# Performance work log

Hardware: AMD Instinct MI355X
Metric: run time of the kernel (lower is better)

## Reference

```python
import jax, jax.numpy as jnp
import numpy as np

BN_EPS = 1e-5

def conv1x1(x, w, b):
    # x: [B, Cin, L], w: [Cout, Cin], b: [Cout] -> [B, Cout, L]
    return jnp.einsum('bcl,oc->bol', x, w) + b[None, :, None]

def maxpool2(x):
    # x: [B, C, L] -> [B, C, L//2], kernel=stride=2
    B, C, L = x.shape
    return x.reshape(B, C, L // 2, 2).max(axis=-1)

def setup_inputs() -> dict:
    key = jax.random.key(0)
    ks = jax.random.split(key, 12)
    B, C, L = 8, 512, 4096
    Ci = C // 2
    s_in = 1.0 / np.sqrt(C)
    s_mid = 1.0 / np.sqrt(Ci)
    return {
        'x':       jax.random.normal(ks[0], (B, C, L), jnp.float32),
        'theta_w': jax.random.uniform(ks[1], (Ci, C), jnp.float32, -s_in, s_in),
        'theta_b': jax.random.uniform(ks[2], (Ci,), jnp.float32, -s_in, s_in),
        'phi_w':   jax.random.uniform(ks[3], (Ci, C), jnp.float32, -s_in, s_in),
        'phi_b':   jax.random.uniform(ks[4], (Ci,), jnp.float32, -s_in, s_in),
        'g_w':     jax.random.uniform(ks[5], (Ci, C), jnp.float32, -s_in, s_in),
        'g_b':     jax.random.uniform(ks[6], (Ci,), jnp.float32, -s_in, s_in),
        'wz_w':    jax.random.uniform(ks[7], (C, Ci), jnp.float32, -s_mid, s_mid),
        'wz_b':    jax.random.uniform(ks[8], (C,), jnp.float32, -s_mid, s_mid),
        'bn_gamma': jax.random.normal(ks[9], (C,), jnp.float32),
        'bn_beta':  jax.random.normal(ks[10], (C,), jnp.float32),
    }

def reference(x, theta_w, theta_b, phi_w, phi_b, g_w, g_b, wz_w, wz_b, bn_gamma, bn_beta):
    B, C, L = x.shape
    Ci = C // 2
    # projections
    theta = conv1x1(x, theta_w, theta_b)                 # [B, Ci, L]
    phi   = maxpool2(conv1x1(x, phi_w, phi_b))           # [B, Ci, L/2]
    g     = maxpool2(conv1x1(x, g_w, g_b))               # [B, Ci, L/2]
    # non-local attention (unscaled)
    f = jnp.einsum('bcq,bck->bqk', theta, phi)           # [B, L, L/2]
    f = jax.nn.softmax(f, axis=-1)
    y = jnp.einsum('bqk,bck->bcq', f, g)                 # [B, Ci, L]
    # wz: conv1x1 + BatchNorm1d (training mode: batch stats, biased var)
    z = conv1x1(y, wz_w, wz_b)                           # [B, C, L]
    mean = z.mean(axis=(0, 2))
    var = ((z - mean[None, :, None]) ** 2).mean(axis=(0, 2))
    z_hat = (z - mean[None, :, None]) * jax.lax.rsqrt(var + BN_EPS)[None, :, None]
    wz = z_hat * bn_gamma[None, :, None] + bn_beta[None, :, None]
    return wz + x
```

## Files before the change

### kernel.cpp

```cpp
#include <hip/hip_runtime.h>

#define BATCH 8
#define CIN   512
#define LEN   4096
#define CI    256
#define KLEN  2048

typedef _Float16 half_t;
typedef _Float16 half2_t __attribute__((ext_vector_type(2)));
typedef _Float16 half4_t __attribute__((ext_vector_type(4)));
typedef _Float16 half8_t __attribute__((ext_vector_type(8)));
typedef float    floatx4 __attribute__((ext_vector_type(4)));

__device__ __forceinline__ void async16(void* lds_dst, const void* g_src) {
    __builtin_amdgcn_global_load_lds(
        (const __attribute__((address_space(1))) unsigned int*)g_src,
        (__attribute__((address_space(3))) unsigned int*)lds_dst,
        16, 0, 0);
}

__global__ __launch_bounds__(256) void xpose_kernel(
    const float* __restrict__ x, half_t* __restrict__ xhT)
{
    __shared__ half_t tile[64][72];
    const int b = blockIdx.z, c0 = blockIdx.y * 64, l0 = blockIdx.x * 64;
    const int t = threadIdx.x;
    #pragma unroll
    for (int i = 0; i < 4; i++) {
        int fid = t + 256 * i;
        int c = fid >> 4, lb = (fid & 15) << 2;
        float4 v = *(const float4*)(x + ((size_t)b * CIN + c0 + c) * LEN + l0 + lb);
        tile[lb + 0][c] = (half_t)v.x;
        tile[lb + 1][c] = (half_t)v.y;
        tile[lb + 2][c] = (half_t)v.z;
        tile[lb + 3][c] = (half_t)v.w;
    }
    __syncthreads();
    #pragma unroll
    for (int i = 0; i < 2; i++) {
        int fid = t + 256 * i;
        int l = fid >> 3, cb = (fid & 7) << 3;
        half8_t v = *(const half8_t*)&tile[l][cb];
        *(half8_t*)(xhT + ((size_t)b * LEN + l0 + l) * CIN + c0 + cb) = v;
    }
}

__global__ __launch_bounds__(256) void wconv_kernel(
    const float* __restrict__ tw, const float* __restrict__ pw,
    const float* __restrict__ gw, const float* __restrict__ wzw,
    half_t* __restrict__ Wh, half_t* __restrict__ wzh)
{
    size_t base = ((size_t)blockIdx.x * 256 + threadIdx.x) * 8;
    const float* src;
    half_t* dst;
    if (base < 768 * 512) {
        size_t o = base >> 9, c = base & 511;
        src = (o < 256 ? tw + o * 512
                       : (o < 512 ? pw + (o - 256) * 512 : gw + (o - 512) * 512)) + c;
        dst = Wh + base;
    } else {
        size_t off = base - 768 * 512;
        src = wzw + off;
        dst = wzh + off;
    }
    float4 a = *(const float4*)src, b2 = *(const float4*)(src + 4);
    half8_t h = { (half_t)a.x, (half_t)a.y, (half_t)a.z, (half_t)a.w,
                  (half_t)b2.x, (half_t)b2.y, (half_t)b2.z, (half_t)b2.w };
    *(half8_t*)dst = h;
}

__global__ __launch_bounds__(256, 2) void projmm_kernel(
    const half_t* __restrict__ xhT, const half_t* __restrict__ Wh,
    const float* __restrict__ tb, const float* __restrict__ pb,
    const float* __restrict__ gb,
    half_t* __restrict__ thetaT, half_t* __restrict__ phiT,
    half_t* __restrict__ gH)
{
    __shared__ half_t wsm[128 * 32];
    __shared__ half_t xsm[128 * 32];

    const int b  = blockIdx.z;
    const int o0 = blockIdx.y * 128;
    const int l0 = blockIdx.x * 128;
    const int t  = threadIdx.x;
    const int lane = t & 63, w = t >> 6;
    const int ln = lane & 15, quad = lane >> 4;
    const int wm = w >> 1, wn = w & 1;

    floatx4 acc[4][4];
    #pragma unroll
    for (int mi = 0; mi < 4; mi++)
        #pragma unroll
        for (int nj = 0; nj < 4; nj++) acc[mi][nj] = (floatx4)(0.0f);

    const half_t* Wb = Wh + (size_t)o0 * 512;
    const half_t* xb = xhT + ((size_t)b * LEN + l0) * CIN;

    for (int k0 = 0; k0 < 512; k0 += 32) {
        __syncthreads();
        #pragma unroll
        for (int it = 0; it < 2; it++) {
            int off = t * 16 + it * 4096;
            int row = off >> 6, c8 = (off >> 4) & 3;
            async16(&wsm[off >> 1], Wb + (size_t)row * 512 + k0 + c8 * 8);
            async16(&xsm[off >> 1], xb + (size_t)row * CIN + k0 + c8 * 8);
        }
        __syncthreads();
        half8_t af[4], bf[4];
        #pragma unroll
        for (int mi = 0; mi < 4; mi++)
            af[mi] = *(const half8_t*)&wsm[(wm * 64 + mi * 16 + ln) * 32 + quad * 8];
        #pragma unroll
        for (int nj = 0; nj < 4; nj++)
            bf[nj] = *(const half8_t*)&xsm[(wn * 64 + nj * 16 + ln) * 32 + quad * 8];
        #pragma unroll
        for (int mi = 0; mi < 4; mi++)
            #pragma unroll
            for (int nj = 0; nj < 4; nj++)
                acc[mi][nj] = __builtin_amdgcn_mfma_f32_16x16x32_f16(
                                  af[mi], bf[nj], acc[mi][nj], 0, 0, 0);
    }

    const int which = o0 >> 8;
    const int obase = o0 & 255;
    const float* Bp = which == 0 ? tb : (which == 1 ? pb : gb);

    float bias[4][4];
    #pragma unroll
    for (int mi = 0; mi < 4; mi++)
        #pragma unroll
        for (int r = 0; r < 4; r++)
            bias[mi][r] = Bp[obase + wm * 64 + mi * 16 + quad * 4 + r];

    if (which == 0) {
        #pragma unroll
        for (int mi = 0; mi < 4; mi++) {
            int o = obase + wm * 64 + mi * 16 + quad * 4;
            #pragma unroll
            for (int nj = 0; nj < 4; nj++) {
                int l = l0 + wn * 64 + nj * 16 + ln;
                half4_t v = { (half_t)(acc[mi][nj][0] + bias[mi][0]),
                              (half_t)(acc[mi][nj][1] + bias[mi][1]),
                              (half_t)(acc[mi][nj][2] + bias[mi][2]),
                              (half_t)(acc[mi][nj][3] + bias[mi][3]) };
                *(half4_t*)(thetaT + ((size_t)b * LEN + l) * CI + o) = v;
            }
        }
    } else {
        #pragma unroll
        for (int mi = 0; mi < 4; mi++) {
            int o = obase + wm * 64 + mi * 16 + quad * 4;
            #pragma unroll
            for (int nj = 0; nj < 4; nj++) {
                int l = l0 + wn * 64 + nj * 16 + ln;
                float mx[4];
                #pragma unroll
                for (int r = 0; r < 4; r++) {
                    float other = __shfl_xor(acc[mi][nj][r], 1);
                    mx[r] = fmaxf(acc[mi][nj][r], other) + bias[mi][r];
                }
                if ((ln & 1) == 0) {
                    int kk = l >> 1;
                    if (which == 1) {
                        half4_t v = { (half_t)mx[0], (half_t)mx[1],
                                      (half_t)mx[2], (half_t)mx[3] };
                        *(half4_t*)(phiT + ((size_t)b * KLEN + kk) * CI + o) = v;
                    } else {
                        #pragma unroll
                        for (int r = 0; r < 4; r++)
                            gH[((size_t)b * CI + o + r) * KLEN + kk] = (half_t)mx[r];
                    }
                }
            }
        }
    }
}

__global__ __launch_bounds__(256, 2) void attn_kernel(
    const half_t* __restrict__ thetaT,
    const half_t* __restrict__ phiT,
    const half_t* __restrict__ gH,
    half_t* __restrict__ yhT)
{
    __shared__ half_t phi_s[64 * 256];
    __shared__ half_t g_s[256 * 64];

    const int b    = blockIdx.x;
    const int q0   = blockIdx.y * 64;
    const int t    = threadIdx.x;
    const int w    = t >> 6;
    const int lane = t & 63;
    const int ln   = lane & 15;
    const int quad = lane >> 4;
    const int qw   = q0 + w * 16;

    half8_t thf[8];
    {
        const half_t* thb = thetaT + ((size_t)b * LEN + qw + ln) * CI + quad * 8;
        #pragma unroll
        for (int ch = 0; ch < 8; ch++)
            thf[ch] = *(const half8_t*)(thb + ch * 32);
    }

    floatx4 O[16];
    #pragma unroll
    for (int i = 0; i < 16; i++) O[i] = (floatx4)(0.0f);
    float m_run = -3.0e38f;
    float l_run = 0.0f;

    const half_t* phib = phiT + (size_t)b * KLEN * CI;
    const half_t* gb   = gH   + (size_t)b * CI * KLEN;

    for (int kt = 0; kt < KLEN; kt += 64) {
        __syncthreads();
        #pragma unroll
        for (int it = 0; it < 8; it++) {
            int o   = t * 16 + it * 4096;
            int row = o >> 9;
            int gsw = (o >> 4) & 31;
            int gsrc = gsw ^ (row & 31);
            async16(&phi_s[o >> 1],
                    phib + (size_t)(kt + row) * CI + gsrc * 8);
        }
        #pragma unroll
        for (int it = 0; it < 8; it++) {
            int o   = t * 16 + it * 4096;
            int row = o >> 7;
            int gsw = (o >> 4) & 7;
            int gsrc = gsw ^ (row & 7);
            async16(&g_s[o >> 1],
                    gb + (size_t)row * KLEN + kt + gsrc * 8);
        }
        __syncthreads();

        floatx4 S[4];
        #pragma unroll
        for (int k16 = 0; k16 < 4; k16++) S[k16] = (floatx4)(0.0f);
        #pragma unroll
        for (int k16 = 0; k16 < 4; k16++) {
            int row = k16 * 16 + ln;
            int rs  = row & 31;
            #pragma unroll
            for (int ch = 0; ch < 8; ch++) {
                int gr = (ch * 4 + quad) ^ rs;
                half8_t a = *(const half8_t*)&phi_s[(row << 8) + gr * 8];
                S[k16] = __builtin_amdgcn_mfma_f32_16x16x32_f16(
                             a, thf[ch], S[k16], 0, 0, 0);
            }
        }

        float tmax = S[0][0];
        #pragma unroll
        for (int k16 = 0; k16 < 4; k16++)
            #pragma unroll
            for (int r = 0; r < 4; r++) tmax = fmaxf(tmax, S[k16][r]);
        tmax = fmaxf(tmax, __shfl_xor(tmax, 16));
        tmax = fmaxf(tmax, __shfl_xor(tmax, 32));
        float m_new = fmaxf(m_run, tmax);
        float alpha = __expf(m_run - m_new);
        m_run = m_new;
        l_run *= alpha;

        half4_t P[4];
        #pragma unroll
        for (int k16 = 0; k16 < 4; k16++) {
            float p0 = __expf(S[k16][0] - m_new);
            float p1 = __expf(S[k16][1] - m_new);
            float p2 = __expf(S[k16][2] - m_new);
            float p3 = __expf(S[k16][3] - m_new);
            l_run += (p0 + p1) + (p2 + p3);
            half4_t pv = { (half_t)p0, (half_t)p1, (half_t)p2, (half_t)p3 };
            P[k16] = pv;
        }
        #pragma unroll
        for (int i = 0; i < 16; i++) O[i] *= alpha;

        const int lnm = ln & 7;
        #pragma unroll
        for (int k16 = 0; k16 < 4; k16++) {
            int gr   = (2 * k16 + (quad >> 1)) ^ lnm;
            int coff = gr * 8 + (quad & 1) * 4;
            #pragma unroll
            for (int csub = 0; csub < 16; csub++) {
                int row = csub * 16 + ln;
                half4_t a = *(const half4_t*)&g_s[(row << 6) + coff];
                O[csub] = __builtin_amdgcn_mfma_f32_16x16x16f16(
                              a, P[k16], O[csub], 0, 0, 0);
            }
        }
    }

    l_run += __shfl_xor(l_run, 16);
    l_run += __shfl_xor(l_run, 32);
    float inv = 1.0f / l_run;
    half_t* yb = yhT + ((size_t)b * LEN + qw + ln) * CI;
    #pragma unroll
    for (int csub = 0; csub < 16; csub++) {
        int c = csub * 16 + quad * 4;
        half4_t v = { (half_t)(O[csub][0] * inv), (half_t)(O[csub][1] * inv),
                      (half_t)(O[csub][2] * inv), (half_t)(O[csub][3] * inv) };
        *(half4_t*)(yb + c) = v;
    }
}

__global__ __launch_bounds__(256, 2) void zmm_kernel(
    const half_t* __restrict__ yhT, const half_t* __restrict__ wzh,
    const float* __restrict__ wzb, float* __restrict__ z,
    float* __restrict__ bns, float* __restrict__ bnq)
{
    __shared__ half_t ysm[128 * 32];
    __shared__ half_t wsm[128 * 32];

    const int b  = blockIdx.z;
    const int o0 = blockIdx.y * 128;
    const int l0 = blockIdx.x * 128;
    const int t  = threadIdx.x;
    const int lane = t & 63, w = t >> 6;
    const int ln = lane & 15, quad = lane >> 4;
    const int wm = w >> 1, wn = w & 1;

    floatx4 acc[4][4];
    #pragma unroll
    for (int mi = 0; mi < 4; mi++)
        #pragma unroll
        for (int nj = 0; nj < 4; nj++) acc[mi][nj] = (floatx4)(0.0f);

    const half_t* yb = yhT + ((size_t)b * LEN + l0) * CI;
    const half_t* Wb = wzh + (size_t)o0 * CI;

    for (int k0 = 0; k0 < 256; k0 += 32) {
        __syncthreads();
        #pragma unroll
        for (int it = 0; it < 2; it++) {
            int off = t * 16 + it * 4096;
            int row = off >> 6, c8 = (off >> 4) & 3;
            async16(&ysm[off >> 1], yb + (size_t)row * CI + k0 + c8 * 8);
            async16(&wsm[off >> 1], Wb + (size_t)row * CI + k0 + c8 * 8);
        }
        __syncthreads();
        half8_t af[4], bf[4];
        #pragma unroll
        for (int mi = 0; mi < 4; mi++)
            af[mi] = *(const half8_t*)&ysm[(wm * 64 + mi * 16 + ln) * 32 + quad * 8];
        #pragma unroll
        for (int nj = 0; nj < 4; nj++)
            bf[nj] = *(const half8_t*)&wsm[(wn * 64 + nj * 16 + ln) * 32 + quad * 8];
        #pragma unroll
        for (int mi = 0; mi < 4; mi++)
            #pragma unroll
            for (int nj = 0; nj < 4; nj++)
                acc[mi][nj] = __builtin_amdgcn_mfma_f32_16x16x32_f16(
                                  af[mi], bf[nj], acc[mi][nj], 0, 0, 0);
    }

    float s[4] = {0, 0, 0, 0}, s2[4] = {0, 0, 0, 0};
    #pragma unroll
    for (int nj = 0; nj < 4; nj++) {
        int o = o0 + wn * 64 + nj * 16 + ln;
        float bo = wzb[o];
        #pragma unroll
        for (int mi = 0; mi < 4; mi++) {
            int l = l0 + wm * 64 + mi * 16 + quad * 4;
            float4 v = make_float4(acc[mi][nj][0] + bo, acc[mi][nj][1] + bo,
                                   acc[mi][nj][2] + bo, acc[mi][nj][3] + bo);
            *(float4*)(z + ((size_t)b * CIN + o) * LEN + l) = v;
            s[nj]  += (v.x + v.y) + (v.z + v.w);
            s2[nj] += (v.x * v.x + v.y * v.y) + (v.z * v.z + v.w * v.w);
        }
    }
    #pragma unroll
    for (int nj = 0; nj < 4; nj++) {
        float sv = s[nj], qv = s2[nj];
        sv += __shfl_xor(sv, 16); sv += __shfl_xor(sv, 32);
        qv += __shfl_xor(qv, 16); qv += __shfl_xor(qv, 32);
        if (quad == 0) {
            int o = o0 + wn * 64 + nj * 16 + ln;
            atomicAdd(&bns[o], sv);
            atomicAdd(&bnq[o], qv);
        }
    }
}

__global__ __launch_bounds__(256) void bn_kernel(
    float* __restrict__ z, const float* __restrict__ x,
    const float* __restrict__ bns, const float* __restrict__ bnq,
    const float* __restrict__ gamma, const float* __restrict__ beta)
{
    size_t i4 = (size_t)blockIdx.x * 256 + threadIdx.x;
    size_t base = i4 << 2;
    int c = (int)((base >> 12) & (CIN - 1));
    const float invn = 1.0f / (BATCH * LEN);
    float mean = bns[c] * invn;
    float var  = bnq[c] * invn - mean * mean;
    float sc = gamma[c] * rsqrtf(var + 1e-5f);
    float sh = beta[c] - mean * sc;
    float4 zv = *(const float4*)(z + base);
    float4 xv = *(const float4*)(x + base);
    float4 o;
    o.x = zv.x * sc + sh + xv.x;
    o.y = zv.y * sc + sh + xv.y;
    o.z = zv.z * sc + sh + xv.z;
    o.w = zv.w * sc + sh + xv.w;
    *(float4*)(z + base) = o;
}

extern "C" void kernel_launch(void* const* d_in, const int* in_sizes, int n_in,
                              void* d_out, int out_size, void* d_ws, size_t ws_size,
                              hipStream_t stream)
{
    const float* x     = (const float*)d_in[0];
    const float* tw    = (const float*)d_in[1];
    const float* tb    = (const float*)d_in[2];
    const float* pw    = (const float*)d_in[3];
    const float* pb    = (const float*)d_in[4];
    const float* gw    = (const float*)d_in[5];
    const float* gb    = (const float*)d_in[6];
    const float* wzw   = (const float*)d_in[7];
    const float* wzb   = (const float*)d_in[8];
    const float* gamma = (const float*)d_in[9];
    const float* beta  = (const float*)d_in[10];

    float* out = (float*)d_out;

    half_t* xhT    = (half_t*)d_ws;
    half_t* thetaT = xhT    + (size_t)BATCH * LEN * CIN;
    half_t* phiT   = thetaT + (size_t)BATCH * LEN * CI;
    half_t* gH     = phiT   + (size_t)BATCH * KLEN * CI;
    half_t* yhT    = gH     + (size_t)BATCH * CI * KLEN;
    half_t* Wh     = yhT    + (size_t)BATCH * LEN * CI;
    half_t* wzh    = Wh     + (size_t)768 * 512;
    float*  bns    = (float*)(wzh + (size_t)512 * 256);
    float*  bnq    = bns + CIN;

    hipMemsetAsync(bns, 0, 2 * CIN * sizeof(float), stream);

    wconv_kernel<<<256, 256, 0, stream>>>(tw, pw, gw, wzw, Wh, wzh);

    xpose_kernel<<<dim3(LEN / 64, CIN / 64, BATCH), 256, 0, stream>>>(x, xhT);

    projmm_kernel<<<dim3(LEN / 128, 6, BATCH), 256, 0, stream>>>(
        xhT, Wh, tb, pb, gb, thetaT, phiT, gH);

    attn_kernel<<<dim3(BATCH, LEN / 64), 256, 0, stream>>>(
        thetaT, phiT, gH, yhT);

    zmm_kernel<<<dim3(LEN / 128, CIN / 128, BATCH), 256, 0, stream>>>(
        yhT, wzh, wzb, out, bns, bnq);

    bn_kernel<<<(BATCH * CIN * LEN) / 4 / 256, 256, 0, stream>>>(
        out, x, bns, bnq, gamma, beta);
}
```

Before: 336.8 us.

## Store LDS tiles in MFMA fragment order and permute g for 16x16x32 PV

```diff
diff --git a/kernel.cpp b/kernel.cpp
--- a/kernel.cpp
+++ b/kernel.cpp
@@ -74,7 +74,7 @@
     const float* __restrict__ tb, const float* __restrict__ pb,
     const float* __restrict__ gb,
     half_t* __restrict__ thetaT, half_t* __restrict__ phiT,
-    half_t* __restrict__ gH)
+    half_t* __restrict__ gperm)
 {
     __shared__ half_t wsm[128 * 32];
     __shared__ half_t xsm[128 * 32];
@@ -100,19 +100,20 @@
         __syncthreads();
         #pragma unroll
         for (int it = 0; it < 2; it++) {
-            int off = t * 16 + it * 4096;
-            int row = off >> 6, c8 = (off >> 4) & 3;
-            async16(&wsm[off >> 1], Wb + (size_t)row * 512 + k0 + c8 * 8);
-            async16(&xsm[off >> 1], xb + (size_t)row * CIN + k0 + c8 * 8);
+            int grp = w * 2 + it;
+            async16(&wsm[grp * 512],
+                    Wb + (size_t)(grp * 16 + ln) * 512 + k0 + quad * 8);
+            async16(&xsm[grp * 512],
+                    xb + (size_t)(grp * 16 + ln) * CIN + k0 + quad * 8);
         }
         __syncthreads();
         half8_t af[4], bf[4];
         #pragma unroll
         for (int mi = 0; mi < 4; mi++)
-            af[mi] = *(const half8_t*)&wsm[(wm * 64 + mi * 16 + ln) * 32 + quad * 8];
+            af[mi] = *(const half8_t*)&wsm[(wm * 4 + mi) * 512 + lane * 8];
         #pragma unroll
         for (int nj = 0; nj < 4; nj++)
-            bf[nj] = *(const half8_t*)&xsm[(wn * 64 + nj * 16 + ln) * 32 + quad * 8];
+            bf[nj] = *(const half8_t*)&xsm[(wn * 4 + nj) * 512 + lane * 8];
         #pragma unroll
         for (int mi = 0; mi < 4; mi++)
             #pragma unroll
@@ -166,9 +167,14 @@
                                       (half_t)mx[2], (half_t)mx[3] };
                         *(half4_t*)(phiT + ((size_t)b * KLEN + kk) * CI + o) = v;
                     } else {
+                        int loc = kk & 63;
+                        int v = ((loc >> 5) & 1) * 32 + ((loc >> 2) & 3) * 8
+                              + ((loc >> 4) & 1) * 4 + (loc & 3);
+                        int kdst = (kk & ~63) | v;
                         #pragma unroll
                         for (int r = 0; r < 4; r++)
-                            gH[((size_t)b * CI + o + r) * KLEN + kk] = (half_t)mx[r];
+                            gperm[((size_t)b * CI + o + r) * KLEN + kdst] =
+                                (half_t)mx[r];
                     }
                 }
             }
@@ -179,7 +185,7 @@
 __global__ __launch_bounds__(256, 2) void attn_kernel(
     const half_t* __restrict__ thetaT,
     const half_t* __restrict__ phiT,
-    const half_t* __restrict__ gH,
+    const half_t* __restrict__ gperm,
     half_t* __restrict__ yhT)
 {
     __shared__ half_t phi_s[64 * 256];
@@ -209,27 +215,23 @@
     float l_run = 0.0f;
 
     const half_t* phib = phiT + (size_t)b * KLEN * CI;
-    const half_t* gb   = gH   + (size_t)b * CI * KLEN;
+    const half_t* gpb  = gperm + (size_t)b * CI * KLEN;
 
     for (int kt = 0; kt < KLEN; kt += 64) {
         __syncthreads();
         #pragma unroll
-        for (int it = 0; it < 8; it++) {
-            int o   = t * 16 + it * 4096;
-            int row = o >> 9;
-            int gsw = (o >> 4) & 31;
-            int gsrc = gsw ^ (row & 31);
-            async16(&phi_s[o >> 1],
-                    phib + (size_t)(kt + row) * CI + gsrc * 8);
-        }
-        #pragma unroll
-        for (int it = 0; it < 8; it++) {
-            int o   = t * 16 + it * 4096;
-            int row = o >> 7;
-            int gsw = (o >> 4) & 7;
-            int gsrc = gsw ^ (row & 7);
-            async16(&g_s[o >> 1],
-                    gb + (size_t)row * KLEN + kt + gsrc * 8);
+        for (int ii = 0; ii < 8; ii++) {
+            int grp = w * 8 + ii;
+            int k16 = grp >> 3, ch = grp & 7;
+            async16(&phi_s[grp * 512],
+                    phib + (size_t)(kt + k16 * 16 + ln) * CI + ch * 32 + quad * 8);
+        }
+        #pragma unroll
+        for (int ii = 0; ii < 8; ii++) {
+            int grp = w * 8 + ii;
+            int tc = grp >> 4, csub = grp & 15;
+            async16(&g_s[grp * 512],
+                    gpb + (size_t)(csub * 16 + ln) * KLEN + kt + tc * 32 + quad * 8);
         }
         __syncthreads();
 
@@ -237,17 +239,13 @@
         #pragma unroll
         for (int k16 = 0; k16 < 4; k16++) S[k16] = (floatx4)(0.0f);
         #pragma unroll
-        for (int k16 = 0; k16 < 4; k16++) {
-            int row = k16 * 16 + ln;
-            int rs  = row & 31;
+        for (int k16 = 0; k16 < 4; k16++)
             #pragma unroll
             for (int ch = 0; ch < 8; ch++) {
-                int gr = (ch * 4 + quad) ^ rs;
-                half8_t a = *(const half8_t*)&phi_s[(row << 8) + gr * 8];
+                half8_t a = *(const half8_t*)&phi_s[(k16 * 8 + ch) * 512 + lane * 8];
                 S[k16] = __builtin_amdgcn_mfma_f32_16x16x32_f16(
                              a, thf[ch], S[k16], 0, 0, 0);
             }
-        }
 
         float tmax = S[0][0];
         #pragma unroll
@@ -261,33 +259,35 @@
         m_run = m_new;
         l_run *= alpha;
 
-        half4_t P[4];
+        float p[4][4];
         #pragma unroll
         for (int k16 = 0; k16 < 4; k16++) {
-            float p0 = __expf(S[k16][0] - m_new);
-            float p1 = __expf(S[k16][1] - m_new);
-            float p2 = __expf(S[k16][2] - m_new);
-            float p3 = __expf(S[k16][3] - m_new);
-            l_run += (p0 + p1) + (p2 + p3);
-            half4_t pv = { (half_t)p0, (half_t)p1, (half_t)p2, (half_t)p3 };
-            P[k16] = pv;
+            #pragma unroll
+            for (int r = 0; r < 4; r++) {
+                p[k16][r] = __expf(S[k16][r] - m_new);
+                l_run += p[k16][r];
+            }
+        }
+        half8_t Pf[2];
+        #pragma unroll
+        for (int tc = 0; tc < 2; tc++) {
+            half8_t pv = { (half_t)p[2*tc][0],   (half_t)p[2*tc][1],
+                           (half_t)p[2*tc][2],   (half_t)p[2*tc][3],
+                           (half_t)p[2*tc+1][0], (half_t)p[2*tc+1][1],
+                           (half_t)p[2*tc+1][2], (half_t)p[2*tc+1][3] };
+            Pf[tc] = pv;
         }
         #pragma unroll
         for (int i = 0; i < 16; i++) O[i] *= alpha;
 
-        const int lnm = ln & 7;
-        #pragma unroll
-        for (int k16 = 0; k16 < 4; k16++) {
-            int gr   = (2 * k16 + (quad >> 1)) ^ lnm;
-            int coff = gr * 8 + (quad & 1) * 4;
+        #pragma unroll
+        for (int tc = 0; tc < 2; tc++)
             #pragma unroll
             for (int csub = 0; csub < 16; csub++) {
-                int row = csub * 16 + ln;
-                half4_t a = *(const half4_t*)&g_s[(row << 6) + coff];
-                O[csub] = __builtin_amdgcn_mfma_f32_16x16x16f16(
-                              a, P[k16], O[csub], 0, 0, 0);
+                half8_t a = *(const half8_t*)&g_s[(tc * 16 + csub) * 512 + lane * 8];
+                O[csub] = __builtin_amdgcn_mfma_f32_16x16x32_f16(
+                              a, Pf[tc], O[csub], 0, 0, 0);
             }
-        }
     }
 
     l_run += __shfl_xor(l_run, 16);
@@ -332,19 +332,20 @@
         __syncthreads();
         #pragma unroll
         for (int it = 0; it < 2; it++) {
-            int off = t * 16 + it * 4096;
-            int row = off >> 6, c8 = (off >> 4) & 3;
-            async16(&ysm[off >> 1], yb + (size_t)row * CI + k0 + c8 * 8);
-            async16(&wsm[off >> 1], Wb + (size_t)row * CI + k0 + c8 * 8);
+            int grp = w * 2 + it;
+            async16(&ysm[grp * 512],
+                    yb + (size_t)(grp * 16 + ln) * CI + k0 + quad * 8);
+            async16(&wsm[grp * 512],
+                    Wb + (size_t)(grp * 16 + ln) * CI + k0 + quad * 8);
         }
         __syncthreads();
         half8_t af[4], bf[4];
         #pragma unroll
         for (int mi = 0; mi < 4; mi++)
-            af[mi] = *(const half8_t*)&ysm[(wm * 64 + mi * 16 + ln) * 32 + quad * 8];
+            af[mi] = *(const half8_t*)&ysm[(wm * 4 + mi) * 512 + lane * 8];
         #pragma unroll
         for (int nj = 0; nj < 4; nj++)
-            bf[nj] = *(const half8_t*)&wsm[(wn * 64 + nj * 16 + ln) * 32 + quad * 8];
+            bf[nj] = *(const half8_t*)&wsm[(wn * 4 + nj) * 512 + lane * 8];
         #pragma unroll
         for (int mi = 0; mi < 4; mi++)
             #pragma unroll
@@ -425,8 +426,8 @@
     half_t* xhT    = (half_t*)d_ws;
     half_t* thetaT = xhT    + (size_t)BATCH * LEN * CIN;
     half_t* phiT   = thetaT + (size_t)BATCH * LEN * CI;
-    half_t* gH     = phiT   + (size_t)BATCH * KLEN * CI;
-    half_t* yhT    = gH     + (size_t)BATCH * CI * KLEN;
+    half_t* gperm  = phiT   + (size_t)BATCH * KLEN * CI;
+    half_t* yhT    = gperm  + (size_t)BATCH * CI * KLEN;
     half_t* Wh     = yhT    + (size_t)BATCH * LEN * CI;
     half_t* wzh    = Wh     + (size_t)768 * 512;
     float*  bns    = (float*)(wzh + (size_t)512 * 256);
@@ -439,10 +440,10 @@
     xpose_kernel<<<dim3(LEN / 64, CIN / 64, BATCH), 256, 0, stream>>>(x, xhT);
 
     projmm_kernel<<<dim3(LEN / 128, 6, BATCH), 256, 0, stream>>>(
-        xhT, Wh, tb, pb, gb, thetaT, phiT, gH);
+        xhT, Wh, tb, pb, gb, thetaT, phiT, gperm);
 
     attn_kernel<<<dim3(BATCH, LEN / 64), 256, 0, stream>>>(
-        thetaT, phiT, gH, yhT);
+        thetaT, phiT, gperm, yhT);
 
     zmm_kernel<<<dim3(LEN / 128, CIN / 128, BATCH), 256, 0, stream>>>(
         yhT, wzh, wzb, out, bns, bnq);
```

New measurement: 367.6 us. 9.1% more time.
